# Performance work log

Hardware: AMD Instinct MI355X
Metric: run time of the kernel (lower is better)

The kernel has to match this reference:

```python
import jax, jax.numpy as jnp
import numpy as np

N_EMBD = 1024
N_HEAD = 16
HEAD_SIZE = N_EMBD // N_HEAD
B, T = 2, 2048
LN_EPS = 1e-5


def _layernorm(x, g, b):
    mu = jnp.mean(x, axis=-1, keepdims=True)
    var = jnp.var(x, axis=-1, keepdims=True)
    return (x - mu) * jax.lax.rsqrt(var + LN_EPS) * g + b


def setup_inputs() -> dict:
    key = jax.random.key(0)
    ks = jax.random.split(key, 12)
    s_in = 1.0 / np.sqrt(N_EMBD)
    s_ff = 1.0 / np.sqrt(4 * N_EMBD)
    return {
        "x": jax.random.normal(ks[0], (B, T, N_EMBD), jnp.float32),
        # per-head q/k/v linears stacked head-major: [n_embd, n_embd]
        "Wq": jax.random.uniform(ks[1], (N_EMBD, N_EMBD), jnp.float32, -s_in, s_in),
        "Wk": jax.random.uniform(ks[2], (N_EMBD, N_EMBD), jnp.float32, -s_in, s_in),
        "Wv": jax.random.uniform(ks[3], (N_EMBD, N_EMBD), jnp.float32, -s_in, s_in),
        "Wo": jax.random.uniform(ks[4], (N_EMBD, N_EMBD), jnp.float32, -s_in, s_in),
        "bo": jax.random.uniform(ks[5], (N_EMBD,), jnp.float32, -s_in, s_in),
        "W1": jax.random.uniform(ks[6], (N_EMBD, 4 * N_EMBD), jnp.float32, -s_in, s_in),
        "b1": jax.random.uniform(ks[7], (4 * N_EMBD,), jnp.float32, -s_in, s_in),
        "W2": jax.random.uniform(ks[8], (4 * N_EMBD, N_EMBD), jnp.float32, -s_ff, s_ff),
        "b2": jax.random.uniform(ks[9], (N_EMBD,), jnp.float32, -s_ff, s_ff),
        "g1": jnp.ones((N_EMBD,), jnp.float32),
        "be1": jnp.zeros((N_EMBD,), jnp.float32),
        "g2": jnp.ones((N_EMBD,), jnp.float32),
        "be2": jnp.zeros((N_EMBD,), jnp.float32),
    }


def reference(x, Wq, Wk, Wv, Wo, bo, W1, b1, W2, b2, g1, be1, g2, be2):
    Bx, Tx, C = x.shape
    # --- self-attention on ln1(x) ---
    h = _layernorm(x, g1, be1)
    q = (h @ Wq).reshape(Bx, Tx, N_HEAD, HEAD_SIZE)
    k = (h @ Wk).reshape(Bx, Tx, N_HEAD, HEAD_SIZE)
    v = (h @ Wv).reshape(Bx, Tx, N_HEAD, HEAD_SIZE)
    # NOTE: faithful to source -- scale uses full C (n_embd), not head_size
    scale = C ** (-0.5)
    wei = jnp.einsum("bqhd,bkhd->bhqk", q, k) * scale  # [B,H,T,T]
    causal = jnp.tril(jnp.ones((Tx, Tx), bool))
    wei = jnp.where(causal, wei, -jnp.inf)
    wei = jax.nn.softmax(wei, axis=-1)
    attn = jnp.einsum("bhqk,bkhd->bqhd", wei, v).reshape(Bx, Tx, C)
    x = x + (attn @ Wo + bo)
    # --- feed-forward on ln2(x) ---
    h2 = _layernorm(x, g2, be2)
    x = x + (jax.nn.relu(h2 @ W1 + b1) @ W2 + b2)
    return x
```

## Files before the change

### kernel.cpp

```cpp
#include <hip/hip_runtime.h>
#include <hip/hip_bf16.h>
#include <math.h>

#define BB 2
#define TT 2048
#define CC 1024
#define NH 16
#define HD 64
#define BT (BB*TT)
#define LN_EPS 1e-5f
#define ATT_SCALE 0.03125f

typedef __bf16 bf16x8 __attribute__((ext_vector_type(8)));
typedef __bf16 bf16x4 __attribute__((ext_vector_type(4)));
typedef short shortx4 __attribute__((ext_vector_type(4)));
typedef float floatx4 __attribute__((ext_vector_type(4)));

__device__ __forceinline__ void gl_lds16(const __bf16* g, __bf16* l) {
    __builtin_amdgcn_global_load_lds((const __attribute__((address_space(1))) void*)g,
                                     (__attribute__((address_space(3))) void*)l,
                                     16, 0, 0);
}

#define MFMA32(a, b, c) __builtin_amdgcn_mfma_f32_16x16x32_bf16(a, b, c, 0, 0, 0)

#if __has_builtin(__builtin_amdgcn_mfma_f32_16x16x16_bf16)
__device__ __forceinline__ floatx4 mfma16(bf16x4 a, bf16x4 b, floatx4 c) {
    return __builtin_amdgcn_mfma_f32_16x16x16_bf16(a, b, c, 0, 0, 0);
}
#else
__device__ __forceinline__ floatx4 mfma16(bf16x4 a, bf16x4 b, floatx4 c) {
    return __builtin_amdgcn_mfma_f32_16x16x16bf16_1k(
        __builtin_bit_cast(shortx4, a), __builtin_bit_cast(shortx4, b), c, 0, 0, 0);
}
#endif

#define BARRIER() __builtin_amdgcn_s_barrier()
#define MEMF()  asm volatile("" ::: "memory")
#define LGKM0() asm volatile("s_waitcnt lgkmcnt(0)" ::: "memory")
#define VM4()   asm volatile("s_waitcnt vmcnt(4)" ::: "memory")
#define VM0()   asm volatile("s_waitcnt vmcnt(0)" ::: "memory")

__device__ __forceinline__ void swizzle_xcd(int& xb, int& yb, int& zb) {
    int nx = gridDim.x, ny = gridDim.y;
    int total = nx * ny * (int)gridDim.z;
    int lin = blockIdx.x + nx * (blockIdx.y + ny * blockIdx.z);
    int c = lin & 7, s = lin >> 3;
    int idx = c * (total >> 3) + s;
    xb = idx % nx;
    yb = (idx / nx) % ny;
    zb = idx / (nx * ny);
}

__global__ __launch_bounds__(256) void transpose_ln(
        const float* __restrict__ Wq, const float* __restrict__ Wk,
        const float* __restrict__ Wv, const float* __restrict__ Wo,
        const float* __restrict__ W1, const float* __restrict__ W2,
        __bf16* __restrict__ WqkvT, __bf16* __restrict__ WoT,
        __bf16* __restrict__ W1T, __bf16* __restrict__ W2T,
        const float* __restrict__ x, const float* __restrict__ g1,
        const float* __restrict__ be1, __bf16* __restrict__ hb) {
    __shared__ float t[32][33];
    __shared__ float rs_[4], rss_[4];
    __shared__ float mu_s, inv_s;
    int idx = blockIdx.x;
    if (idx >= 12288) {
        int row = idx - 12288;
        const float4* xr = (const float4*)(x + (size_t)row * CC);
        float4 v = xr[threadIdx.x];
        float s  = v.x + v.y + v.z + v.w;
        float ss = v.x*v.x + v.y*v.y + v.z*v.z + v.w*v.w;
        #pragma unroll
        for (int off = 32; off; off >>= 1) {
            s  += __shfl_down(s, off);
            ss += __shfl_down(ss, off);
        }
        int lane = threadIdx.x & 63, wid = threadIdx.x >> 6;
        if (lane == 0) { rs_[wid] = s; rss_[wid] = ss; }
        __syncthreads();
        if (threadIdx.x == 0) {
            float S  = rs_[0] + rs_[1] + rs_[2] + rs_[3];
            float SS = rss_[0] + rss_[1] + rss_[2] + rss_[3];
            float mu  = S * (1.0f / CC);
            float var = SS * (1.0f / CC) - mu * mu;
            mu_s  = mu;
            inv_s = rsqrtf(var + LN_EPS);
        }
        __syncthreads();
        float mu = mu_s, inv = inv_s;
        float4 gv = ((const float4*)g1)[threadIdx.x];
        float4 bv = ((const float4*)be1)[threadIdx.x];
        bf16x4 o;
        o[0] = (__bf16)((v.x - mu) * inv * gv.x + bv.x);
        o[1] = (__bf16)((v.y - mu) * inv * gv.y + bv.y);
        o[2] = (__bf16)((v.z - mu) * inv * gv.z + bv.z);
        o[3] = (__bf16)((v.w - mu) * inv * gv.w + bv.w);
        *(bf16x4*)(hb + (size_t)row * CC + threadIdx.x * 4) = o;
        return;
    }
    const float* src; __bf16* dst; int K, N, tn, tk;
    if (idx < 3072) {
        int wsel = idx >> 10, local = idx & 1023;
        src = (wsel == 0) ? Wq : (wsel == 1 ? Wk : Wv);
        dst = WqkvT + (size_t)wsel * 1024 * 1024;
        K = 1024; N = 1024; tn = local & 31; tk = local >> 5;
    } else if (idx < 4096) {
        int local = idx - 3072;
        src = Wo; dst = WoT; K = 1024; N = 1024; tn = local & 31; tk = local >> 5;
    } else if (idx < 8192) {
        int local = idx - 4096;
        src = W1; dst = W1T; K = 1024; N = 4096; tn = local & 127; tk = local >> 7;
    } else {
        int local = idx - 8192;
        src = W2; dst = W2T; K = 4096; N = 1024; tn = local & 31; tk = local >> 5;
    }
    int n0 = tn * 32, k0 = tk * 32;
    int tx = threadIdx.x & 31, ty = threadIdx.x >> 5;
    #pragma unroll
    for (int r = ty; r < 32; r += 8)
        t[r][tx] = src[(size_t)(k0 + r) * N + n0 + tx];
    __syncthreads();
    #pragma unroll
    for (int r = ty; r < 32; r += 8)
        dst[(size_t)(n0 + r) * K + k0 + tx] = (__bf16)t[tx][r];
}

__global__ __launch_bounds__(256) void reduce_wo_ln(const __bf16* __restrict__ P,
                                                    const float* __restrict__ bo,
                                                    const float* __restrict__ x,
                                                    const float* __restrict__ g2,
                                                    const float* __restrict__ be2,
                                                    float* __restrict__ x2,
                                                    __bf16* __restrict__ hb) {
    int row = blockIdx.x;
    int c = threadIdx.x * 4;
    const size_t S = (size_t)BT * CC;
    float4 xb = *(const float4*)(x + (size_t)row * CC + c);
    float4 bb = *(const float4*)(bo + c);
    float4 v;
    v.x = xb.x + bb.x;
    v.y = xb.y + bb.y;
    v.z = xb.z + bb.z;
    v.w = xb.w + bb.w;
    #pragma unroll
    for (int z = 0; z < 4; ++z) {
        bf16x4 a = *(const bf16x4*)(P + z * S + (size_t)row * CC + c);
        v.x += (float)a[0]; v.y += (float)a[1]; v.z += (float)a[2]; v.w += (float)a[3];
    }
    *(float4*)(x2 + (size_t)row * CC + c) = v;

    float s  = v.x + v.y + v.z + v.w;
    float ss = v.x*v.x + v.y*v.y + v.z*v.z + v.w*v.w;
    #pragma unroll
    for (int off = 32; off; off >>= 1) {
        s  += __shfl_down(s, off);
        ss += __shfl_down(ss, off);
    }
    __shared__ float rs_[4], rss_[4];
    __shared__ float mu_s, inv_s;
    int lane = threadIdx.x & 63, wid = threadIdx.x >> 6;
    if (lane == 0) { rs_[wid] = s; rss_[wid] = ss; }
    __syncthreads();
    if (threadIdx.x == 0) {
        float S_  = rs_[0] + rs_[1] + rs_[2] + rs_[3];
        float SS = rss_[0] + rss_[1] + rss_[2] + rss_[3];
        float mu  = S_ * (1.0f / CC);
        float var = SS * (1.0f / CC) - mu * mu;
        mu_s  = mu;
        inv_s = rsqrtf(var + LN_EPS);
    }
    __syncthreads();
    float mu = mu_s, inv = inv_s;
    float4 gv = ((const float4*)g2)[threadIdx.x];
    float4 bv = ((const float4*)be2)[threadIdx.x];
    bf16x4 o;
    o[0] = (__bf16)((v.x - mu) * inv * gv.x + bv.x);
    o[1] = (__bf16)((v.y - mu) * inv * gv.y + bv.y);
    o[2] = (__bf16)((v.z - mu) * inv * gv.z + bv.z);
    o[3] = (__bf16)((v.w - mu) * inv * gv.w + bv.w);
    *(bf16x4*)(hb + (size_t)row * CC + c) = o;
}

__global__ __launch_bounds__(256) void reduce_ffn(const __bf16* __restrict__ P,
                                                  const float* __restrict__ b2,
                                                  const float* __restrict__ x2,
                                                  float* __restrict__ out) {
    int row = blockIdx.x;
    int c = threadIdx.x * 4;
    const size_t S = (size_t)BT * CC;
    float4 v = *(const float4*)(x2 + (size_t)row * CC + c);
    float4 bb = *(const float4*)(b2 + c);
    v.x += bb.x; v.y += bb.y; v.z += bb.z; v.w += bb.w;
    #pragma unroll
    for (int z = 0; z < 4; ++z) {
        bf16x4 a = *(const bf16x4*)(P + z * S + (size_t)row * CC + c);
        v.x += (float)a[0]; v.y += (float)a[1]; v.z += (float)a[2]; v.w += (float)a[3];
    }
    *(float4*)(out + (size_t)row * CC + c) = v;
}

__device__ __forceinline__ void stage_half(const __bf16* __restrict__ mat, int row0,
                                           int ldk, int k0, __bf16* lds, int tid) {
    int r = tid >> 3;
    int lch = (tid & 7) ^ (r & 7);
    const __bf16* gp = mat + (size_t)(row0 + r) * ldk + k0 + lch * 8;
    gl_lds16(gp, lds + tid * 8);
    gl_lds16(gp + (size_t)64 * ldk, lds + 4096 + tid * 8);
}

__device__ __forceinline__ void load_a(const __bf16* As_, int qr, int wr, int m, int g,
                                       bf16x8 (&fa)[4][2]) {
    #pragma unroll
    for (int i = 0; i < 4; ++i) {
        int ra = qr * 128 + wr * 64 + i * 16 + m;
        #pragma unroll
        for (int kk = 0; kk < 2; ++kk)
            fa[i][kk] = *(const bf16x8*)&As_[ra * 64 + (((kk * 4 + g) ^ (m & 7)) * 8)];
    }
}

__device__ __forceinline__ void load_b(const __bf16* Bs_, int qc, int wc, int m, int g,
                                       bf16x8 (&fb)[2][2]) {
    #pragma unroll
    for (int j = 0; j < 2; ++j) {
        int rb = qc * 128 + wc * 32 + j * 16 + m;
        #pragma unroll
        for (int kk = 0; kk < 2; ++kk)
            fb[j][kk] = *(const bf16x8*)&Bs_[rb * 64 + (((kk * 4 + g) ^ (m & 7)) * 8)];
    }
}

__device__ __forceinline__ void mfma_q(bf16x8 (&fa)[4][2], bf16x8 (&fb)[2][2],
                                       floatx4 (&a)[4][2]) {
    __builtin_amdgcn_s_setprio(1);
    #pragma unroll
    for (int i = 0; i < 4; ++i)
        #pragma unroll
        for (int j = 0; j < 2; ++j)
            #pragma unroll
            for (int kk = 0; kk < 2; ++kk)
                a[i][j] = MFMA32(fa[i][kk], fb[j][kk], a[i][j]);
    __builtin_amdgcn_s_setprio(0);
}

template<int SK, typename OT, bool BIAS, bool RELU, bool VSPLIT>
__global__ __launch_bounds__(512, 2) void gemm256(const __bf16* __restrict__ A,
                                                  const __bf16* __restrict__ Bt,
                                                  const float* __restrict__ bias,
                                                  OT* __restrict__ C,
                                                  __bf16* __restrict__ vt,
                                                  int M, int N, int K) {
    __shared__ __bf16 As[2][16384];
    __shared__ __bf16 Bs[2][16384];
    int bx, by, bz;
    swizzle_xcd(bx, by, bz);
    const int tid = threadIdx.x;
    const int l = tid & 63, w = tid >> 6;
    const int m = l & 15, g = l >> 4;
    const int wr = w >> 2, wc = w & 3;
    const int m0 = by * 256, n0 = bx * 256;
    const int Keff = K / SK;
    const int kb = (SK > 1) ? bz * Keff : 0;
    const int iters = Keff >> 7;

    floatx4 acc[2][2][4][2];
    #pragma unroll
    for (int a = 0; a < 2; ++a)
        #pragma unroll
        for (int b = 0; b < 2; ++b)
            #pragma unroll
            for (int i = 0; i < 4; ++i)
                #pragma unroll
                for (int j = 0; j < 2; ++j) {
                    floatx4 z = {0.f, 0.f, 0.f, 0.f};
                    acc[a][b][i][j] = z;
                }

    stage_half(A,  m0,       K, kb,      &As[0][0],    tid);
    stage_half(Bt, n0,       K, kb,      &Bs[0][0],    tid);
    stage_half(Bt, n0 + 128, K, kb,      &Bs[0][8192], tid);
    stage_half(A,  m0 + 128, K, kb,      &As[0][8192], tid);
    stage_half(A,  m0,       K, kb + 64, &As[1][0],    tid);
    stage_half(Bt, n0 + 128, K, kb + 64, &Bs[1][8192], tid);
    VM4(); BARRIER(); MEMF();

    bf16x8 fa[4][2], fbA[2][2], fbB[2][2];

    for (int it = 0; it < iters; ++it) {
        const bool lastI = (it == iters - 1);
        const int kB = kb + (2 * it + 1) * 64;
        const int kC = kB + 64;
        const int kD = kC + 64;

        load_a(&As[0][0], 0, wr, m, g, fa);
        load_b(&Bs[0][0], 0, wc, m, g, fbA);
        stage_half(Bt, n0, K, kB, &Bs[1][0], tid);
        BARRIER(); LGKM0(); mfma_q(fa, fbA, acc[0][0]); BARRIER(); MEMF();
        load_b(&Bs[0][0], 1, wc, m, g, fbB);
        stage_half(A, m0 + 128, K, kB, &As[1][8192], tid);
        BARRIER(); LGKM0(); mfma_q(fa, fbB, acc[0][1]); BARRIER(); MEMF();
        load_a(&As[0][0], 1, wr, m, g, fa);
        if (!lastI) stage_half(A, m0, K, kC, &As[0][0], tid);
        BARRIER(); LGKM0(); mfma_q(fa, fbB, acc[1][1]); BARRIER(); MEMF();
        if (!lastI) { stage_half(Bt, n0 + 128, K, kC, &Bs[0][8192], tid);
                      VM4(); }
        else VM0();
        BARRIER(); mfma_q(fa, fbA, acc[1][0]); BARRIER(); MEMF();

        load_a(&As[1][0], 0, wr, m, g, fa);
        load_b(&Bs[1][0], 0, wc, m, g, fbA);
        if (!lastI) stage_half(Bt, n0, K, kC, &Bs[0][0], tid);
        BARRIER(); LGKM0(); mfma_q(fa, fbA, acc[0][0]); BARRIER(); MEMF();
        load_b(&Bs[1][0], 1, wc, m, g, fbB);
        if (!lastI) stage_half(A, m0 + 128, K, kC, &As[0][8192], tid);
        BARRIER(); LGKM0(); mfma_q(fa, fbB, acc[0][1]); BARRIER(); MEMF();
        load_a(&As[1][0], 1, wr, m, g, fa);
        if (!lastI) stage_half(A, m0, K, kD, &As[1][0], tid);
        BARRIER(); LGKM0(); mfma_q(fa, fbB, acc[1][1]); BARRIER(); MEMF();
        if (!lastI) { stage_half(Bt, n0 + 128, K, kD, &Bs[1][8192], tid);
                      VM4(); }
        BARRIER(); mfma_q(fa, fbA, acc[1][0]); BARRIER(); MEMF();
    }

    if (SK > 1) {
        __bf16* P = (__bf16*)C + (size_t)bz * M * N;
        #pragma unroll
        for (int qr = 0; qr < 2; ++qr)
            #pragma unroll
            for (int i = 0; i < 4; ++i) {
                int row = m0 + qr * 128 + wr * 64 + i * 16 + g * 4;
                #pragma unroll
                for (int qc = 0; qc < 2; ++qc)
                    #pragma unroll
                    for (int j = 0; j < 2; ++j) {
                        int col = n0 + qc * 128 + wc * 32 + j * 16 + m;
                        #pragma unroll
                        for (int r = 0; r < 4; ++r)
                            P[(size_t)(row + r) * N + col] = (__bf16)acc[qr][qc][i][j][r];
                    }
            }
    } else if (VSPLIT && n0 >= 2048) {
        #pragma unroll
        for (int qr = 0; qr < 2; ++qr)
            #pragma unroll
            for (int i = 0; i < 4; ++i) {
                int row = m0 + qr * 128 + wr * 64 + i * 16 + g * 4;
                int bb = row >> 11, t0 = row & 2047;
                #pragma unroll
                for (int qc = 0; qc < 2; ++qc)
                    #pragma unroll
                    for (int j = 0; j < 2; ++j) {
                        int cv = n0 + qc * 128 + wc * 32 + j * 16 + m - 2048;
                        bf16x4 o;
                        #pragma unroll
                        for (int r = 0; r < 4; ++r) o[r] = (__bf16)acc[qr][qc][i][j][r];
                        *(bf16x4*)(vt + ((size_t)(bb * NH + (cv >> 6)) * HD + (cv & 63)) * 2048 + t0) = o;
                    }
            }
    } else {
        #pragma unroll
        for (int qr = 0; qr < 2; ++qr)
            #pragma unroll
            for (int i = 0; i < 4; ++i) {
                int row = m0 + qr * 128 + wr * 64 + i * 16 + g * 4;
                #pragma unroll
                for (int qc = 0; qc < 2; ++qc)
                    #pragma unroll
                    for (int j = 0; j < 2; ++j) {
                        int col = n0 + qc * 128 + wc * 32 + j * 16 + m;
                        float bv = BIAS ? bias[col] : 0.0f;
                        #pragma unroll
                        for (int r = 0; r < 4; ++r) {
                            float vo = acc[qr][qc][i][j][r] + bv;
                            if (RELU) vo = fmaxf(vo, 0.0f);
                            C[(size_t)(row + r) * N + col] = (OT)vo;
                        }
                    }
            }
    }
}

__global__ __launch_bounds__(256, 2) void attn_mfma3(const __bf16* __restrict__ qkv,
                                                     const __bf16* __restrict__ vt,
                                                     __bf16* __restrict__ att) {
    const int lin = blockIdx.x;
    const int half = lin >> 8, pid = lin & 255;
    const int q0 = pid & 7, h = (pid >> 3) & 15, b = pid >> 7;
    const int qt = half ? 15 - q0 : q0;

    const int tid = threadIdx.x;
    const int l = tid & 63, w = tid >> 6;
    const int m = l & 15, g = l >> 4;

    __shared__ __bf16 Ks[2][128][32];
    __shared__ __bf16 Vt3[8][64][16];

    const __bf16* qp = qkv + (size_t)b * TT * 3072 + h * HD;
    const __bf16* kp = qp + 1024;
    const __bf16* vh = vt + (size_t)(b * NH + h) * HD * 2048;

    bf16x8 qb[2][2];
    #pragma unroll
    for (int nt = 0; nt < 2; ++nt) {
        int qrow = qt * 128 + w * 32 + nt * 16 + m;
        qb[nt][0] = *(const bf16x8*)(qp + (size_t)qrow * 3072 + g * 8);
        qb[nt][1] = *(const bf16x8*)(qp + (size_t)qrow * 3072 + 32 + g * 8);
    }

    floatx4 O[2][4];
    float l_s[2] = {0.0f, 0.0f};
    #pragma unroll
    for (int nt = 0; nt < 2; ++nt)
        #pragma unroll
        for (int jd = 0; jd < 4; ++jd) {
            floatx4 z = {0.f, 0.f, 0.f, 0.f};
            O[nt][jd] = z;
        }

    for (int kt = 0; kt <= qt; ++kt) {
        __syncthreads();
        #pragma unroll
        for (int c = 0; c < 4; ++c) {
            int idx = w * 4 + c;
            int dh = idx >> 3, k16 = idx & 7;
            gl_lds16(kp + (size_t)(kt * 128 + k16 * 16 + (l >> 2)) * 3072
                        + dh * 32 + (((l & 3) ^ ((l >> 3) & 3)) * 8),
                     (__bf16*)Ks + dh * 4096 + k16 * 512);
        }
        #pragma unroll
        for (int c = 0; c < 4; ++c) {
            int idx = w * 4 + c;
            int jt = idx >> 1, dhf = idx & 1;
            gl_lds16(vh + (size_t)(dhf * 32 + (l >> 1)) * 2048 + kt * 128
                        + jt * 16 + (((l & 1) ^ ((l >> 3) & 1)) * 8),
                     (__bf16*)Vt3 + jt * 1024 + dhf * 512);
        }
        __syncthreads();

        floatx4 S[2][8];
        #pragma unroll
        for (int jt = 0; jt < 8; ++jt) {
            int co = (g ^ ((m >> 1) & 3)) * 8;
            bf16x8 kf0 = *(const bf16x8*)&Ks[0][jt * 16 + m][co];
            bf16x8 kf1 = *(const bf16x8*)&Ks[1][jt * 16 + m][co];
            #pragma unroll
            for (int nt = 0; nt < 2; ++nt) {
                floatx4 z = {0.f, 0.f, 0.f, 0.f};
                z = MFMA32(kf0, qb[nt][0], z);
                S[nt][jt] = MFMA32(kf1, qb[nt][1], z);
            }
        }

        bf16x4 pv[2][8];
        const bool last = (kt == qt);
        #pragma unroll
        for (int nt = 0; nt < 2; ++nt) {
            if (last) {
                int qr = w * 32 + nt * 16 + m;
                #pragma unroll
                for (int jt = 0; jt < 8; ++jt)
                    #pragma unroll
                    for (int r = 0; r < 4; ++r)
                        if (jt * 16 + g * 4 + r > qr) S[nt][jt][r] = -1e30f;
            }
            float ls = 0.0f;
            #pragma unroll
            for (int jt = 0; jt < 8; ++jt) {
                bf16x4 t;
                #pragma unroll
                for (int r = 0; r < 4; ++r) {
                    float p = __expf(S[nt][jt][r] * ATT_SCALE);
                    ls += p;
                    t[r] = (__bf16)p;
                }
                pv[nt][jt] = t;
            }
            l_s[nt] += ls;
        }

        #pragma unroll
        for (int jt = 0; jt < 8; ++jt)
            #pragma unroll
            for (int jd = 0; jd < 4; ++jd) {
                bf16x4 vf = *(const bf16x4*)&Vt3[jt][jd * 16 + m]
                                [((g >> 1) ^ ((m >> 2) & 1)) * 8 + (g & 1) * 4];
                #pragma unroll
                for (int nt = 0; nt < 2; ++nt)
                    O[nt][jd] = mfma16(vf, pv[nt][jt], O[nt][jd]);
            }
    }

    #pragma unroll
    for (int nt = 0; nt < 2; ++nt) {
        float lsum = l_s[nt];
        lsum += __shfl_xor(lsum, 16, 64);
        lsum += __shfl_xor(lsum, 32, 64);
        float inv = 1.0f / lsum;
        int qrow = qt * 128 + w * 32 + nt * 16 + m;
        #pragma unroll
        for (int jd = 0; jd < 4; ++jd) {
            bf16x4 o;
            #pragma unroll
            for (int r = 0; r < 4; ++r) o[r] = (__bf16)(O[nt][jd][r] * inv);
            *(bf16x4*)(att + ((size_t)b * TT + qrow) * CC + h * HD + jd * 16 + g * 4) = o;
        }
    }
}

extern "C" void kernel_launch(void* const* d_in, const int* in_sizes, int n_in,
                              void* d_out, int out_size, void* d_ws, size_t ws_size,
                              hipStream_t stream) {
    const float* x   = (const float*)d_in[0];
    const float* Wq  = (const float*)d_in[1];
    const float* Wk  = (const float*)d_in[2];
    const float* Wv  = (const float*)d_in[3];
    const float* Wo  = (const float*)d_in[4];
    const float* bo  = (const float*)d_in[5];
    const float* W1  = (const float*)d_in[6];
    const float* b1  = (const float*)d_in[7];
    const float* W2  = (const float*)d_in[8];
    const float* b2  = (const float*)d_in[9];
    const float* g1  = (const float*)d_in[10];
    const float* be1 = (const float*)d_in[11];
    const float* g2  = (const float*)d_in[12];
    const float* be2 = (const float*)d_in[13];
    float* out = (float*)d_out;

    char* p = (char*)d_ws;
    char*   pool  = p;          p += (size_t)32 * 1024 * 1024;
    __bf16* qkvb  = (__bf16*)pool;
    __bf16* vtb   = (__bf16*)(pool + (size_t)BT * 3072 * 2);
    __bf16* wop   = (__bf16*)pool;
    __bf16* ffp   = (__bf16*)pool;
    __bf16* attb  = (__bf16*)p; p += (size_t)BT * CC * 2;
    __bf16* hb    = (__bf16*)p; p += (size_t)BT * CC * 2;
    float*  x2    = (float*)p;  p += (size_t)BT * CC * 4;
    __bf16* ffb   = (__bf16*)p; p += (size_t)BT * 4096 * 2;
    __bf16* WqkvT = (__bf16*)p; p += (size_t)3072 * 1024 * 2;
    __bf16* WoT   = (__bf16*)p; p += (size_t)1024 * 1024 * 2;
    __bf16* W1T   = (__bf16*)p; p += (size_t)4096 * 1024 * 2;
    __bf16* W2T   = (__bf16*)p; p += (size_t)1024 * 4096 * 2;

    transpose_ln<<<16384, 256, 0, stream>>>(Wq, Wk, Wv, Wo, W1, W2,
                                            WqkvT, WoT, W1T, W2T,
                                            x, g1, be1, hb);
    gemm256<1, __bf16, false, false, true><<<dim3(12, 16), 512, 0, stream>>>(
        hb, WqkvT, nullptr, qkvb, vtb, BT, 3072, 1024);
    attn_mfma3<<<512, 256, 0, stream>>>(qkvb, vtb, attb);
    gemm256<4, __bf16, false, false, false><<<dim3(4, 16, 4), 512, 0, stream>>>(
        attb, WoT, nullptr, wop, nullptr, BT, 1024, 1024);
    reduce_wo_ln<<<BT, 256, 0, stream>>>(wop, bo, x, g2, be2, x2, hb);
    gemm256<1, __bf16, true, true, false><<<dim3(16, 16), 512, 0, stream>>>(
        hb, W1T, b1, ffb, nullptr, BT, 4096, 1024);
    gemm256<4, __bf16, false, false, false><<<dim3(4, 16, 4), 512, 0, stream>>>(
        ffb, W2T, nullptr, ffp, nullptr, BT, 1024, 4096);
    reduce_ffn<<<BT, 256, 0, stream>>>(ffp, b2, x2, out);
}
```

Before: 329.2 us.

## Double-buffer K/V tiles in attention kernel and raise MFMA wave priority

The attention kernel now keeps two LDS buffers for K and V and issues the global-to-LDS loads for the next key tile before computing on the current one, with a single wait and barrier at the end of each iteration. The K tile layout becomes row-major 64-wide with an XOR swizzle, and s_setprio raises wave priority around the MFMA sections. This is meant to hide global load latency behind the QK and PV matrix work. It doubles LDS use per block (64 KB with two blocks per CU), which may limit occupancy, and it depends on the barrier ordering being right to avoid overwriting a buffer that is still being read.

```diff
diff --git a/kernel.cpp b/kernel.cpp
--- a/kernel.cpp
+++ b/kernel.cpp
@@ -380,7 +380,7 @@
     }
 }
 
-__global__ __launch_bounds__(256, 2) void attn_mfma3(const __bf16* __restrict__ qkv,
+__global__ __launch_bounds__(256, 2) void attn_mfma4(const __bf16* __restrict__ qkv,
                                                      const __bf16* __restrict__ vt,
                                                      __bf16* __restrict__ att) {
     const int lin = blockIdx.x;
@@ -392,12 +392,32 @@
     const int l = tid & 63, w = tid >> 6;
     const int m = l & 15, g = l >> 4;
 
-    __shared__ __bf16 Ks[2][128][32];
-    __shared__ __bf16 Vt3[8][64][16];
+    __shared__ __bf16 Ks[2][8192];
+    __shared__ __bf16 Vs[2][8192];
 
     const __bf16* qp = qkv + (size_t)b * TT * 3072 + h * HD;
     const __bf16* kp = qp + 1024;
     const __bf16* vh = vt + (size_t)(b * NH + h) * HD * 2048;
+
+    const int sr  = tid >> 3;
+    const int sch = (tid & 7) ^ (sr & 7);
+
+#define STAGE_KV(buf, ktile)                                                       \
+    {                                                                              \
+        const __bf16* gk = kp + (size_t)((ktile) * 128 + sr) * 3072 + sch * 8;     \
+        gl_lds16(gk,                     &Ks[buf][0]    + tid * 8);                \
+        gl_lds16(gk + (size_t)32 * 3072, &Ks[buf][2048] + tid * 8);                \
+        gl_lds16(gk + (size_t)64 * 3072, &Ks[buf][4096] + tid * 8);                \
+        gl_lds16(gk + (size_t)96 * 3072, &Ks[buf][6144] + tid * 8);                \
+        _Pragma("unroll")                                                          \
+        for (int c = 0; c < 4; ++c) {                                              \
+            int idx = w * 4 + c;                                                   \
+            int jt = idx >> 1, dhf = idx & 1;                                      \
+            gl_lds16(vh + (size_t)(dhf * 32 + (l >> 1)) * 2048 + (ktile) * 128     \
+                        + jt * 16 + (((l & 1) ^ ((l >> 3) & 1)) * 8),              \
+                     &Vs[buf][0] + jt * 1024 + dhf * 512);                         \
+        }                                                                          \
+    }
 
     bf16x8 qb[2][2];
     #pragma unroll
@@ -417,32 +437,22 @@
             O[nt][jd] = z;
         }
 
+    STAGE_KV(0, 0);
+    VM0(); BARRIER(); MEMF();
+
     for (int kt = 0; kt <= qt; ++kt) {
-        __syncthreads();
-        #pragma unroll
-        for (int c = 0; c < 4; ++c) {
-            int idx = w * 4 + c;
-            int dh = idx >> 3, k16 = idx & 7;
-            gl_lds16(kp + (size_t)(kt * 128 + k16 * 16 + (l >> 2)) * 3072
-                        + dh * 32 + (((l & 3) ^ ((l >> 3) & 3)) * 8),
-                     (__bf16*)Ks + dh * 4096 + k16 * 512);
-        }
-        #pragma unroll
-        for (int c = 0; c < 4; ++c) {
-            int idx = w * 4 + c;
-            int jt = idx >> 1, dhf = idx & 1;
-            gl_lds16(vh + (size_t)(dhf * 32 + (l >> 1)) * 2048 + kt * 128
-                        + jt * 16 + (((l & 1) ^ ((l >> 3) & 1)) * 8),
-                     (__bf16*)Vt3 + jt * 1024 + dhf * 512);
-        }
-        __syncthreads();
+        const int cur = kt & 1;
+        if (kt < qt) STAGE_KV(cur ^ 1, kt + 1);
+        const __bf16* Kb = &Ks[cur][0];
+        const __bf16* Vb = &Vs[cur][0];
 
         floatx4 S[2][8];
+        __builtin_amdgcn_s_setprio(1);
         #pragma unroll
         for (int jt = 0; jt < 8; ++jt) {
-            int co = (g ^ ((m >> 1) & 3)) * 8;
-            bf16x8 kf0 = *(const bf16x8*)&Ks[0][jt * 16 + m][co];
-            bf16x8 kf1 = *(const bf16x8*)&Ks[1][jt * 16 + m][co];
+            int rk = (jt * 16 + m) * 64;
+            bf16x8 kf0 = *(const bf16x8*)&Kb[rk + ((g ^ (m & 7)) * 8)];
+            bf16x8 kf1 = *(const bf16x8*)&Kb[rk + (((4 + g) ^ (m & 7)) * 8)];
             #pragma unroll
             for (int nt = 0; nt < 2; ++nt) {
                 floatx4 z = {0.f, 0.f, 0.f, 0.f};
@@ -450,6 +460,7 @@
                 S[nt][jt] = MFMA32(kf1, qb[nt][1], z);
             }
         }
+        __builtin_amdgcn_s_setprio(0);
 
         bf16x4 pv[2][8];
         const bool last = (kt == qt);
@@ -478,16 +489,20 @@
             l_s[nt] += ls;
         }
 
+        __builtin_amdgcn_s_setprio(1);
         #pragma unroll
         for (int jt = 0; jt < 8; ++jt)
             #pragma unroll
             for (int jd = 0; jd < 4; ++jd) {
-                bf16x4 vf = *(const bf16x4*)&Vt3[jt][jd * 16 + m]
-                                [((g >> 1) ^ ((m >> 2) & 1)) * 8 + (g & 1) * 4];
+                bf16x4 vf = *(const bf16x4*)&Vb[jt * 1024 + (jd * 16 + m) * 16
+                                + (((g >> 1) ^ ((m >> 2) & 1)) * 8 + (g & 1) * 4)];
                 #pragma unroll
                 for (int nt = 0; nt < 2; ++nt)
                     O[nt][jd] = mfma16(vf, pv[nt][jt], O[nt][jd]);
             }
+        __builtin_amdgcn_s_setprio(0);
+
+        if (kt < qt) { VM0(); BARRIER(); MEMF(); }
     }
 
     #pragma unroll
@@ -505,6 +520,7 @@
             *(bf16x4*)(att + ((size_t)b * TT + qrow) * CC + h * HD + jd * 16 + g * 4) = o;
         }
     }
+#undef STAGE_KV
 }
 
 extern "C" void kernel_launch(void* const* d_in, const int* in_sizes, int n_in,
@@ -546,7 +562,7 @@
                                             x, g1, be1, hb);
     gemm256<1, __bf16, false, false, true><<<dim3(12, 16), 512, 0, stream>>>(
         hb, WqkvT, nullptr, qkvb, vtb, BT, 3072, 1024);
-    attn_mfma3<<<512, 256, 0, stream>>>(qkvb, vtb, attb);
+    attn_mfma4<<<512, 256, 0, stream>>>(qkvb, vtb, attb);
     gemm256<4, __bf16, false, false, false><<<dim3(4, 16, 4), 512, 0, stream>>>(
         attb, WoT, nullptr, wop, nullptr, BT, 1024, 1024);
     reduce_wo_ln<<<BT, 256, 0, stream>>>(wop, bo, x, g2, be2, x2, hb);
```

Measured after the change: 334.7 us. No clear change (+1.7%).

## Halve attention query tile to 64 rows and fold scale into Q projection

Applied to the files above, without the earlier changes.

The attention kernel now gives each block 64 query rows (16 per wave) instead of 128, which doubles the grid to 1024 blocks and raises the occupancy hint to 4 blocks per CU. The causal K/V loop ends at the 128-key tile that covers the query tile, and the mask is applied only on that last tile. The softmax scale is moved out of the attention inner loop and into the QKV GEMM epilogue, where Q columns are multiplied by the scale. The aim is finer load balance and more waves in flight. In exchange, each K/V tile loaded into LDS is reused by half as many query rows, so K/V load traffic rises, and part of the last tile is computed and then masked.

```diff
diff --git a/kernel.cpp b/kernel.cpp
--- a/kernel.cpp
+++ b/kernel.cpp
@@ -373,6 +373,7 @@
                         for (int r = 0; r < 4; ++r) {
                             float vo = acc[qr][qc][i][j][r] + bv;
                             if (RELU) vo = fmaxf(vo, 0.0f);
+                            if (VSPLIT && col < 1024) vo *= ATT_SCALE;
                             C[(size_t)(row + r) * N + col] = (OT)vo;
                         }
                     }
@@ -380,13 +381,12 @@
     }
 }
 
-__global__ __launch_bounds__(256, 2) void attn_mfma3(const __bf16* __restrict__ qkv,
+__global__ __launch_bounds__(256, 4) void attn_mfma5(const __bf16* __restrict__ qkv,
                                                      const __bf16* __restrict__ vt,
                                                      __bf16* __restrict__ att) {
     const int lin = blockIdx.x;
-    const int half = lin >> 8, pid = lin & 255;
-    const int q0 = pid & 7, h = (pid >> 3) & 15, b = pid >> 7;
-    const int qt = half ? 15 - q0 : q0;
+    const int q0 = lin & 15, h = (lin >> 4) & 15, b = (lin >> 8) & 1, half = lin >> 9;
+    const int qs = half ? 31 - q0 : q0;
 
     const int tid = threadIdx.x;
     const int l = tid & 63, w = tid >> 6;
@@ -399,25 +399,20 @@
     const __bf16* kp = qp + 1024;
     const __bf16* vh = vt + (size_t)(b * NH + h) * HD * 2048;
 
-    bf16x8 qb[2][2];
-    #pragma unroll
-    for (int nt = 0; nt < 2; ++nt) {
-        int qrow = qt * 128 + w * 32 + nt * 16 + m;
-        qb[nt][0] = *(const bf16x8*)(qp + (size_t)qrow * 3072 + g * 8);
-        qb[nt][1] = *(const bf16x8*)(qp + (size_t)qrow * 3072 + 32 + g * 8);
-    }
-
-    floatx4 O[2][4];
-    float l_s[2] = {0.0f, 0.0f};
-    #pragma unroll
-    for (int nt = 0; nt < 2; ++nt)
-        #pragma unroll
-        for (int jd = 0; jd < 4; ++jd) {
-            floatx4 z = {0.f, 0.f, 0.f, 0.f};
-            O[nt][jd] = z;
-        }
-
-    for (int kt = 0; kt <= qt; ++kt) {
+    bf16x8 qb0, qb1;
+    {
+        int qrow = qs * 64 + w * 16 + m;
+        qb0 = *(const bf16x8*)(qp + (size_t)qrow * 3072 + g * 8);
+        qb1 = *(const bf16x8*)(qp + (size_t)qrow * 3072 + 32 + g * 8);
+    }
+
+    floatx4 O[4];
+    float l_s = 0.0f;
+    #pragma unroll
+    for (int jd = 0; jd < 4; ++jd) { floatx4 z = {0.f, 0.f, 0.f, 0.f}; O[jd] = z; }
+
+    const int ktmax = qs >> 1;
+    for (int kt = 0; kt <= ktmax; ++kt) {
         __syncthreads();
         #pragma unroll
         for (int c = 0; c < 4; ++c) {
@@ -437,45 +432,37 @@
         }
         __syncthreads();
 
-        floatx4 S[2][8];
+        floatx4 S[8];
         #pragma unroll
         for (int jt = 0; jt < 8; ++jt) {
             int co = (g ^ ((m >> 1) & 3)) * 8;
             bf16x8 kf0 = *(const bf16x8*)&Ks[0][jt * 16 + m][co];
             bf16x8 kf1 = *(const bf16x8*)&Ks[1][jt * 16 + m][co];
-            #pragma unroll
-            for (int nt = 0; nt < 2; ++nt) {
-                floatx4 z = {0.f, 0.f, 0.f, 0.f};
-                z = MFMA32(kf0, qb[nt][0], z);
-                S[nt][jt] = MFMA32(kf1, qb[nt][1], z);
+            floatx4 z = {0.f, 0.f, 0.f, 0.f};
+            z = MFMA32(kf0, qb0, z);
+            S[jt] = MFMA32(kf1, qb1, z);
+        }
+
+        const bool last = (kt == ktmax);
+        if (last) {
+            int qr = (qs & 1) * 64 + w * 16 + m;
+            #pragma unroll
+            for (int jt = 0; jt < 8; ++jt)
+                #pragma unroll
+                for (int r = 0; r < 4; ++r)
+                    if (jt * 16 + g * 4 + r > qr) S[jt][r] = -1e30f;
+        }
+        bf16x4 pv[8];
+        #pragma unroll
+        for (int jt = 0; jt < 8; ++jt) {
+            bf16x4 t;
+            #pragma unroll
+            for (int r = 0; r < 4; ++r) {
+                float p = __expf(S[jt][r]);
+                l_s += p;
+                t[r] = (__bf16)p;
             }
-        }
-
-        bf16x4 pv[2][8];
-        const bool last = (kt == qt);
-        #pragma unroll
-        for (int nt = 0; nt < 2; ++nt) {
-            if (last) {
-                int qr = w * 32 + nt * 16 + m;
-                #pragma unroll
-                for (int jt = 0; jt < 8; ++jt)
-                    #pragma unroll
-                    for (int r = 0; r < 4; ++r)
-                        if (jt * 16 + g * 4 + r > qr) S[nt][jt][r] = -1e30f;
-            }
-            float ls = 0.0f;
-            #pragma unroll
-            for (int jt = 0; jt < 8; ++jt) {
-                bf16x4 t;
-                #pragma unroll
-                for (int r = 0; r < 4; ++r) {
-                    float p = __expf(S[nt][jt][r] * ATT_SCALE);
-                    ls += p;
-                    t[r] = (__bf16)p;
-                }
-                pv[nt][jt] = t;
-            }
-            l_s[nt] += ls;
+            pv[jt] = t;
         }
 
         #pragma unroll
@@ -484,26 +471,21 @@
             for (int jd = 0; jd < 4; ++jd) {
                 bf16x4 vf = *(const bf16x4*)&Vt3[jt][jd * 16 + m]
                                 [((g >> 1) ^ ((m >> 2) & 1)) * 8 + (g & 1) * 4];
-                #pragma unroll
-                for (int nt = 0; nt < 2; ++nt)
-                    O[nt][jd] = mfma16(vf, pv[nt][jt], O[nt][jd]);
+                O[jd] = mfma16(vf, pv[jt], O[jd]);
             }
     }
 
-    #pragma unroll
-    for (int nt = 0; nt < 2; ++nt) {
-        float lsum = l_s[nt];
-        lsum += __shfl_xor(lsum, 16, 64);
-        lsum += __shfl_xor(lsum, 32, 64);
-        float inv = 1.0f / lsum;
-        int qrow = qt * 128 + w * 32 + nt * 16 + m;
-        #pragma unroll
-        for (int jd = 0; jd < 4; ++jd) {
-            bf16x4 o;
-            #pragma unroll
-            for (int r = 0; r < 4; ++r) o[r] = (__bf16)(O[nt][jd][r] * inv);
-            *(bf16x4*)(att + ((size_t)b * TT + qrow) * CC + h * HD + jd * 16 + g * 4) = o;
-        }
+    float lsum = l_s;
+    lsum += __shfl_xor(lsum, 16, 64);
+    lsum += __shfl_xor(lsum, 32, 64);
+    float inv = 1.0f / lsum;
+    int qrow = qs * 64 + w * 16 + m;
+    #pragma unroll
+    for (int jd = 0; jd < 4; ++jd) {
+        bf16x4 o;
+        #pragma unroll
+        for (int r = 0; r < 4; ++r) o[r] = (__bf16)(O[jd][r] * inv);
+        *(bf16x4*)(att + ((size_t)b * TT + qrow) * CC + h * HD + jd * 16 + g * 4) = o;
     }
 }
 
@@ -546,7 +528,7 @@
                                             x, g1, be1, hb);
     gemm256<1, __bf16, false, false, true><<<dim3(12, 16), 512, 0, stream>>>(
         hb, WqkvT, nullptr, qkvb, vtb, BT, 3072, 1024);
-    attn_mfma3<<<512, 256, 0, stream>>>(qkvb, vtb, attb);
+    attn_mfma5<<<1024, 256, 0, stream>>>(qkvb, vtb, attb);
     gemm256<4, __bf16, false, false, false><<<dim3(4, 16, 4), 512, 0, stream>>>(
         attb, WoT, nullptr, wop, nullptr, BT, 1024, 1024);
     reduce_wo_ln<<<BT, 256, 0, stream>>>(wop, bo, x, g2, be2, x2, hb);
```

New measurement: 321.8 us. 1.02x faster.
